# Kernel tuning notes

Measured on AMD Instinct MI355X. Metric: run time of the kernel, lower is better.

## Reference

```python
import jax, jax.numpy as jnp
import numpy as np
from jax import lax

# dims (see shape_source)
B, T = 256, 32
DQ, K, S, CTX = 128, 8, 4, 16
D = 2 * DQ + 1            # state_flat = [q (DQ), p (DQ), extra (1)]
EVO, DT, DAMP, TAU = 8, 0.2, 0.1, 1.0
TOPK = 2
GAMMA = 10.0              # gamma_pred
EPS = 1e-8


def _router(q, ctx, Wq, Wc, b):
    # chart routing: softmax over K charts, temperature TAU
    return jax.nn.softmax((q @ Wq + ctx @ Wc + b) / TAU, axis=-1)


def _decode_topk(x, w, rw, rb):
    # x: [B,D], w: [B,K] chart weights -> [B,S] logits via top-k chart mixture
    logits_k = jnp.einsum('bd,kvd->bkv', x, rw) + rb          # [B,K,S]
    wv, idx = lax.top_k(w, TOPK)
    wn = wv / jnp.clip(wv.sum(-1, keepdims=True), EPS)
    wm = jnp.zeros_like(w).at[jnp.arange(w.shape[0])[:, None], idx].set(wn)
    return jnp.einsum('bkv,bk->bv', logits_k, wm)


def setup_inputs() -> dict:
    key = jax.random.key(0)
    ks = jax.random.split(key, 11)
    return {
        'inputs': jax.random.randint(ks[0], (B, T), 0, 2),
        'targets': jax.random.randint(ks[1], (B, T), 0, S),
        'task_ids': jax.random.randint(ks[2], (B, T), 0, 2),
        'initial_state_flat': jax.random.normal(ks[3], (B, D), jnp.float32),
        'bit_embed': jax.random.normal(ks[4], (2, DQ), jnp.float32),
        'task_u_embed': jax.random.normal(ks[5], (2, DQ), jnp.float32),
        'router_ctx_embed': jax.random.normal(ks[6], (2, CTX), jnp.float32),
        'readout_weight': 0.1 * jax.random.normal(ks[7], (K, S, D), jnp.float32),
        'readout_bias': jnp.zeros((K, S), jnp.float32),
        'router_Wq': 0.1 * jax.random.normal(ks[8], (DQ, K), jnp.float32),
        'router_Wc': 0.1 * jax.random.normal(ks[9], (CTX, K), jnp.float32),
        'router_b': jnp.zeros((K,), jnp.float32),
        'A': 0.02 * jax.random.normal(ks[10], (K, DQ, DQ), jnp.float32),
    }


def reference(inputs, targets, task_ids, initial_state_flat, bit_embed, task_u_embed,
              router_ctx_embed, readout_weight, readout_bias, router_Wq, router_Wc,
              router_b, A):
    Bn, Tn = inputs.shape
    rows = jnp.arange(Bn)
    targets_prev = jnp.concatenate([jnp.zeros_like(targets[:, :1]), targets[:, :-1]], axis=1)

    def step(carry, xs):
        state, tF, tacc, tce, usage, tsum, tcnt, scw, scnt = carry
        bit_t, target_t, prev_t, task_t = xs
        u = jnp.tanh(bit_embed[bit_t]) + jnp.tanh(task_u_embed[task_t])   # [B,DQ]
        ctx = jnp.tanh(router_ctx_embed[task_t])                          # [B,CTX]

        def evo(st, _):
            q, p, s = st[:, :DQ], st[:, DQ:2 * DQ], st[:, 2 * DQ:]
            w = _router(q, ctx, router_Wq, router_Wc, router_b)           # [B,K]
            # chart-weighted mixture-of-experts dynamics (semi-implicit, damped)
            force = jnp.einsum('bk,kij,bj->bi', w, A, jnp.tanh(q))
            p_new = (1.0 - DT * DAMP) * p + DT * (force + u)
            q_new = q + DT * jnp.tanh(p_new)
            return jnp.concatenate([q_new, p_new, s], axis=1), w

        state, ws = lax.scan(evo, state, None, length=EVO)
        chart_w = ws[-1]                                                  # router w from last evo step
        q = state[:, :DQ]
        chart_w_next = _router(q, ctx, router_Wq, router_Wc, router_b)
        logits = _decode_topk(state, chart_w_next, readout_weight, readout_bias)  # [B,S]
        logits2 = logits[:, :2]
        tgt2 = jnp.where(task_t == 0, target_t, 0)
        ce2 = -jax.nn.log_softmax(logits2, axis=-1)[rows, tgt2]
        ce4 = -jax.nn.log_softmax(logits, axis=-1)[rows, target_t]
        mask2 = (task_t == 0).astype(jnp.float32)
        pred_error = mask2 * ce2 + (1.0 - mask2) * ce4
        chart_state_loss = -jnp.log(jnp.clip(chart_w, EPS))[rows, prev_t]
        F_t = GAMMA * (pred_error + chart_state_loss)

        pred = jnp.where(task_t == 0, jnp.argmax(logits2, -1), jnp.argmax(logits, -1))
        correct = (pred == target_t).astype(jnp.float32)
        task_oh = jax.nn.one_hot(task_t, 2, dtype=jnp.float32)
        mask4 = (task_t == 1).astype(jnp.float32)[:, None]
        state_oh = jax.nn.one_hot(prev_t, S, dtype=jnp.float32)
        carry = (state,
                 tF + F_t.mean(),
                 tacc + correct.mean(),
                 tce + pred_error.mean(),
                 usage + chart_w.sum(0),
                 tsum + (correct[:, None] * task_oh).sum(0),
                 tcnt + task_oh.sum(0),
                 scw + (state_oh * mask4).T @ chart_w,
                 scnt + (state_oh * mask4).sum(0))
        return carry, None

    zf = jnp.zeros((), jnp.float32)
    init = (initial_state_flat, zf, zf, zf,
            jnp.zeros((K,), jnp.float32), jnp.zeros((2,), jnp.float32),
            jnp.zeros((2,), jnp.float32), jnp.zeros((S, K), jnp.float32),
            jnp.zeros((S,), jnp.float32))
    xs = (inputs.T, targets.T, targets_prev.T, task_ids.T)
    (state, tF, tacc, tce, usage, tsum, tcnt, scw, scnt), _ = lax.scan(step, init, xs)

    mean_F = tF / Tn
    mean_acc = tacc / Tn
    mean_ce = tce / Tn
    per_task_acc = tsum / (tcnt + EPS)
    dist = usage / (usage.sum() + EPS)
    chart_ent = -(dist * jnp.log(dist + EPS)).sum()
    joint = scw / (scw.sum() + EPS)
    p_s = joint.sum(1, keepdims=True)
    p_c = joint.sum(0, keepdims=True)
    mi = (joint * (jnp.log(joint + EPS) - jnp.log(p_s + EPS) - jnp.log(p_c + EPS))).sum()
    mi = jnp.where(scw.sum() > 0, jnp.clip(mi, 0.0), 0.0)
    return (mean_F, mean_acc, mean_ce, usage, chart_ent, per_task_acc, scw, scnt, mi)
```

## Files before the change

### kernel.cpp

```cpp
#include <hip/hip_runtime.h>
#include <hip/hip_fp16.h>

namespace {
constexpr int kT = 32, kDQ = 128, kK = 8, kS = 4, kCTX = 16, kD = 257, kEVO = 8;
constexpr float kDT = 0.2f, kDAMP = 0.1f, kGAMMA = 10.0f, kEPS = 1e-8f;

typedef _Float16 h2 __attribute__((ext_vector_type(2)));

__device__ __forceinline__ float dot2h(unsigned a, unsigned b, float c) {
#if __has_builtin(__builtin_amdgcn_fdot2)
  return __builtin_amdgcn_fdot2(__builtin_bit_cast(h2, a), __builtin_bit_cast(h2, b), c, false);
#else
  h2 ha = __builtin_bit_cast(h2, a), hb = __builtin_bit_cast(h2, b);
  return c + (float)ha.x * (float)hb.x + (float)ha.y * (float)hb.y;
#endif
}

__device__ __forceinline__ unsigned packh2(float lo, float hi) {
  __half l = __float2half(lo), h = __float2half(hi);
  return (unsigned)__half_as_ushort(l) | ((unsigned)__half_as_ushort(h) << 16);
}
}

extern "C" __global__ void __launch_bounds__(1024)
seq_main(const int* __restrict__ inputs, const int* __restrict__ targets,
         const int* __restrict__ task_ids, const float* __restrict__ st0,
         const float* __restrict__ bit_emb, const float* __restrict__ task_u,
         const float* __restrict__ ctx_emb, const float* __restrict__ rw_g,
         const float* __restrict__ rb_g, const float* __restrict__ Wq_g,
         const float* __restrict__ Wc_g, const float* __restrict__ b_g,
         const float* __restrict__ A_g, float* __restrict__ ws) {
  const int tid = threadIdx.x;
  const int b = blockIdx.x;
  const int kq = tid >> 7, iq = tid & 127;

  __shared__ __align__(16) float q_l[kDQ];
  __shared__ __align__(16) float p_l[kDQ];
  __shared__ __align__(16) float u4_l[4][kDQ];
  __shared__ __align__(16) unsigned tq_l[kDQ / 2];
  __shared__ __align__(16) float Ybuf[kK][kDQ];
  __shared__ __align__(16) float Wq_l[kK][kDQ];
  __shared__ float wq_ctx2[2][kK];
  __shared__ float wlog_l[kK];
  __shared__ float w_l[kK];
  __shared__ float chartw_l[kK];
  __shared__ float rw_l[kK * kS * kD];
  __shared__ float rb_l[kK * kS];
  __shared__ float lk_l[kK * kS];
  __shared__ float acc_l[64];
  __shared__ float s_l;

  for (int idx = tid; idx < kK * kS * kD; idx += 1024) rw_l[idx] = rw_g[idx];
  if (tid < kDQ * kK) { int j = tid >> 3, kk = tid & 7; Wq_l[kk][j] = Wq_g[tid]; }
  if (tid < kK * kS) rb_l[tid] = rb_g[tid];
  if (tid < kDQ) { q_l[tid] = st0[b * kD + tid]; p_l[tid] = st0[b * kD + kDQ + tid]; }
  if (tid == 0) s_l = st0[b * kD + 2 * kDQ];
  if (tid < 64) acc_l[tid] = 0.f;
  if (tid < 512) {
    int cb = tid >> 7, i = tid & 127;
    u4_l[cb][i] = tanhf(bit_emb[(cb & 1) * kDQ + i]) + tanhf(task_u[(cb >> 1) * kDQ + i]);
  }
  if (tid < 16) {
    int tk = tid >> 3, kk = tid & 7;
    float s = b_g[kk];
    #pragma unroll
    for (int c = 0; c < kCTX; c++) s += tanhf(ctx_emb[tk * kCTX + c]) * Wc_g[c * kK + kk];
    wq_ctx2[tk][kk] = s;
  }
  unsigned a_[64];
  {
    const float4* Arow = reinterpret_cast<const float4*>(A_g + ((size_t)(kq * kDQ + iq)) * kDQ);
    #pragma unroll
    for (int jj = 0; jj < 32; jj++) {
      float4 f = Arow[jj];
      a_[2 * jj] = packh2(f.x, f.y);
      a_[2 * jj + 1] = packh2(f.z, f.w);
    }
  }
  __syncthreads();

  if (tid < kDQ) {
    float tv = tanhf(q_l[tid]);
    float to = __shfl_xor(tv, 1);
    if (!(tid & 1)) tq_l[tid >> 1] = packh2(tv, to);
  }
  if (tid < 512) {
    int kk = tid >> 6, l = tid & 63;
    float2 qp = reinterpret_cast<const float2*>(q_l)[l];
    float2 wp = reinterpret_cast<const float2*>(&Wq_l[kk][0])[l];
    float part = qp.x * wp.x + qp.y * wp.y;
    part += __shfl_xor(part, 1);  part += __shfl_xor(part, 2);
    part += __shfl_xor(part, 4);  part += __shfl_xor(part, 8);
    part += __shfl_xor(part, 16); part += __shfl_xor(part, 32);
    if (l == 0) wlog_l[kk] = part;
  }
  __syncthreads();

  const int boff = b * kT;
  for (int t = 0; t < kT; t++) {
    const int bit = inputs[boff + t];
    const int task = task_ids[boff + t];
    const int uix = task * 2 + bit;

    for (int e = 0; e < kEVO; e++) {
      if (tid < kK) {
        float myl = wlog_l[tid] + wq_ctx2[task][tid];
        float mx = myl;
        #pragma unroll
        for (int kk = 0; kk < kK; kk++) mx = fmaxf(mx, wlog_l[kk] + wq_ctx2[task][kk]);
        float ev = expf(myl - mx);
        float sm = ev;
        sm += __shfl_xor(sm, 1); sm += __shfl_xor(sm, 2); sm += __shfl_xor(sm, 4);
        w_l[tid] = ev / sm;
      }
      float y = 0.f;
      {
        const uint4* tq4 = reinterpret_cast<const uint4*>(tq_l);
        #pragma unroll
        for (int jj = 0; jj < 16; jj++) {
          uint4 tt = tq4[jj];
          y = dot2h(a_[4 * jj + 0], tt.x, y);
          y = dot2h(a_[4 * jj + 1], tt.y, y);
          y = dot2h(a_[4 * jj + 2], tt.z, y);
          y = dot2h(a_[4 * jj + 3], tt.w, y);
        }
      }
      Ybuf[kq][iq] = y;
      __syncthreads();
      if (tid < kDQ) {
        float f = 0.f;
        #pragma unroll
        for (int kk = 0; kk < kK; kk++) f += w_l[kk] * Ybuf[kk][tid];
        float pv = (1.f - kDT * kDAMP) * p_l[tid] + kDT * (f + u4_l[uix][tid]);
        float qv = q_l[tid] + kDT * tanhf(pv);
        p_l[tid] = pv; q_l[tid] = qv;
        float tv = tanhf(qv);
        float to = __shfl_xor(tv, 1);
        if (!(tid & 1)) tq_l[tid >> 1] = packh2(tv, to);
        if (e == kEVO - 1 && tid < kK) chartw_l[tid] = w_l[tid];
      }
      __syncthreads();
      if (tid < 512) {
        int kk = tid >> 6, l = tid & 63;
        float2 qp = reinterpret_cast<const float2*>(q_l)[l];
        float2 wp = reinterpret_cast<const float2*>(&Wq_l[kk][0])[l];
        float part = qp.x * wp.x + qp.y * wp.y;
        part += __shfl_xor(part, 1);  part += __shfl_xor(part, 2);
        part += __shfl_xor(part, 4);  part += __shfl_xor(part, 8);
        part += __shfl_xor(part, 16); part += __shfl_xor(part, 32);
        if (l == 0) wlog_l[kk] = part;
      }
      __syncthreads();
    }

    {
      int pair = tid >> 5, ln = tid & 31;
      const float* rwrow = &rw_l[pair * kD];
      float sacc = 0.f;
      #pragma unroll
      for (int m = 0; m < 8; m++) {
        int d = ln + 32 * m;
        float sv = (m < 4) ? q_l[d] : p_l[d - kDQ];
        sacc += sv * rwrow[d];
      }
      if (ln == 0) sacc += s_l * rwrow[256];
      sacc += __shfl_xor(sacc, 1); sacc += __shfl_xor(sacc, 2);
      sacc += __shfl_xor(sacc, 4); sacc += __shfl_xor(sacc, 8);
      sacc += __shfl_xor(sacc, 16);
      if (ln == 0) lk_l[pair] = sacc + rb_l[pair];
    }
    __syncthreads();
    if (tid == 0) {
      const int tgt = targets[boff + t];
      const int prv = (t == 0) ? 0 : targets[boff + t - 1];
      float lg[kK]; float mx = -1e30f;
      #pragma unroll
      for (int kk = 0; kk < kK; kk++) { lg[kk] = wlog_l[kk] + wq_ctx2[task][kk]; mx = fmaxf(mx, lg[kk]); }
      float cw[kK]; float ssum = 0.f;
      #pragma unroll
      for (int kk = 0; kk < kK; kk++) { cw[kk] = expf(lg[kk] - mx); ssum += cw[kk]; }
      float invs = 1.f / ssum;
      #pragma unroll
      for (int kk = 0; kk < kK; kk++) cw[kk] *= invs;
      int i0 = 0; float v0 = cw[0];
      #pragma unroll
      for (int kk = 1; kk < kK; kk++) if (cw[kk] > v0) { v0 = cw[kk]; i0 = kk; }
      int i1 = (i0 == 0) ? 1 : 0; float v1 = cw[i1];
      #pragma unroll
      for (int kk = 0; kk < kK; kk++) if (kk != i0 && cw[kk] > v1) { v1 = cw[kk]; i1 = kk; }
      float wsum = fmaxf(v0 + v1, kEPS);
      float wn0 = v0 / wsum, wn1 = v1 / wsum;
      float lg4[4];
      #pragma unroll
      for (int v = 0; v < 4; v++) lg4[v] = wn0 * lk_l[i0 * 4 + v] + wn1 * lk_l[i1 * 4 + v];
      float m2 = fmaxf(lg4[0], lg4[1]);
      float lse2 = m2 + logf(expf(lg4[0] - m2) + expf(lg4[1] - m2));
      float m4 = fmaxf(fmaxf(lg4[0], lg4[1]), fmaxf(lg4[2], lg4[3]));
      float lse4 = m4 + logf(expf(lg4[0] - m4) + expf(lg4[1] - m4) + expf(lg4[2] - m4) + expf(lg4[3] - m4));
      int idx2 = (tgt < 1) ? tgt : 1;
      float p2 = (idx2 == 0) ? lg4[0] : lg4[1];
      float p4 = (tgt == 0) ? lg4[0] : ((tgt == 1) ? lg4[1] : ((tgt == 2) ? lg4[2] : lg4[3]));
      float ce2 = lse2 - p2, ce4 = lse4 - p4;
      float pe = (task == 0) ? ce2 : ce4;
      int pred;
      if (task == 0) pred = (lg4[1] > lg4[0]) ? 1 : 0;
      else {
        pred = 0; float bv = lg4[0];
        if (lg4[1] > bv) { bv = lg4[1]; pred = 1; }
        if (lg4[2] > bv) { bv = lg4[2]; pred = 2; }
        if (lg4[3] > bv) { bv = lg4[3]; pred = 3; }
      }
      float corr = (pred == tgt) ? 1.f : 0.f;
      float csl = -logf(fmaxf(chartw_l[prv], kEPS));
      float Ft = kGAMMA * (pe + csl);
      acc_l[0] += Ft; acc_l[1] += corr; acc_l[2] += pe;
      #pragma unroll
      for (int kk = 0; kk < kK; kk++) acc_l[3 + kk] += chartw_l[kk];
      acc_l[11 + task] += corr; acc_l[13 + task] += 1.f;
      if (task == 1) {
        #pragma unroll
        for (int kk = 0; kk < kK; kk++) acc_l[15 + prv * kK + kk] += chartw_l[kk];
        acc_l[47 + prv] += 1.f;
      }
    }
    __syncthreads();
  }

  __syncthreads();
  if (tid < 64) ws[b * 64 + tid] = acc_l[tid];
}

extern "C" __global__ void seq_finalize(const float* __restrict__ ws, float* __restrict__ out) {
  const int tid = threadIdx.x;
  __shared__ float red[51];
  if (tid < 51) {
    float s = 0.f;
    for (int b = 0; b < 256; b++) s += ws[b * 64 + tid];
    red[tid] = s;
  }
  __syncthreads();
  if (tid == 0) {
    const float BT = 256.f * 32.f;
    out[0] = red[0] / BT;
    out[1] = red[1] / BT;
    out[2] = red[2] / BT;
    float us = 0.f;
    for (int k = 0; k < 8; k++) { out[3 + k] = red[3 + k]; us += red[3 + k]; }
    float ent = 0.f;
    for (int k = 0; k < 8; k++) {
      float dist = red[3 + k] / (us + kEPS);
      ent -= dist * logf(dist + kEPS);
    }
    out[11] = ent;
    out[12] = red[11] / (red[13] + kEPS);
    out[13] = red[12] / (red[14] + kEPS);
    float tot = 0.f;
    for (int j = 0; j < 32; j++) { out[14 + j] = red[15 + j]; tot += red[15 + j]; }
    for (int s2 = 0; s2 < 4; s2++) out[46 + s2] = red[47 + s2];
    float inv = 1.f / (tot + kEPS);
    float ps[4] = {0.f, 0.f, 0.f, 0.f};
    float pc[8] = {0.f, 0.f, 0.f, 0.f, 0.f, 0.f, 0.f, 0.f};
    for (int s2 = 0; s2 < 4; s2++)
      for (int k = 0; k < 8; k++) {
        float jv = red[15 + s2 * 8 + k] * inv;
        ps[s2] += jv; pc[k] += jv;
      }
    float mi = 0.f;
    for (int s2 = 0; s2 < 4; s2++)
      for (int k = 0; k < 8; k++) {
        float jv = red[15 + s2 * 8 + k] * inv;
        mi += jv * (logf(jv + kEPS) - logf(ps[s2] + kEPS) - logf(pc[k] + kEPS));
      }
    mi = (tot > 0.f) ? fmaxf(mi, 0.f) : 0.f;
    out[50] = mi;
  }
}

extern "C" void kernel_launch(void* const* d_in, const int* in_sizes, int n_in,
                              void* d_out, int out_size, void* d_ws, size_t ws_size,
                              hipStream_t stream) {
  (void)in_sizes; (void)n_in; (void)out_size; (void)ws_size;
  const int* inputs   = (const int*)d_in[0];
  const int* targets  = (const int*)d_in[1];
  const int* task_ids = (const int*)d_in[2];
  const float* st0      = (const float*)d_in[3];
  const float* bit_emb  = (const float*)d_in[4];
  const float* task_u   = (const float*)d_in[5];
  const float* ctx_emb  = (const float*)d_in[6];
  const float* rw       = (const float*)d_in[7];
  const float* rb       = (const float*)d_in[8];
  const float* Wq       = (const float*)d_in[9];
  const float* Wc       = (const float*)d_in[10];
  const float* bb       = (const float*)d_in[11];
  const float* A        = (const float*)d_in[12];
  float* ws  = (float*)d_ws;
  float* out = (float*)d_out;
  hipLaunchKernelGGL(seq_main, dim3(256), dim3(1024), 0, stream,
                     inputs, targets, task_ids, st0, bit_emb, task_u, ctx_emb,
                     rw, rb, Wq, Wc, bb, A, ws);
  hipLaunchKernelGGL(seq_finalize, dim3(1), dim3(64), 0, stream, ws, out);
}
```

Measured before the change: 441.6 us.

## Compute chart force matvecs with MFMA and keep per-lane state in registers

```diff
diff --git a/kernel.cpp b/kernel.cpp
--- a/kernel.cpp
+++ b/kernel.cpp
@@ -5,20 +5,17 @@
 constexpr int kT = 32, kDQ = 128, kK = 8, kS = 4, kCTX = 16, kD = 257, kEVO = 8;
 constexpr float kDT = 0.2f, kDAMP = 0.1f, kGAMMA = 10.0f, kEPS = 1e-8f;
 
-typedef _Float16 h2 __attribute__((ext_vector_type(2)));
-
-__device__ __forceinline__ float dot2h(unsigned a, unsigned b, float c) {
-#if __has_builtin(__builtin_amdgcn_fdot2)
-  return __builtin_amdgcn_fdot2(__builtin_bit_cast(h2, a), __builtin_bit_cast(h2, b), c, false);
-#else
-  h2 ha = __builtin_bit_cast(h2, a), hb = __builtin_bit_cast(h2, b);
-  return c + (float)ha.x * (float)hb.x + (float)ha.y * (float)hb.y;
-#endif
-}
+typedef _Float16 half8 __attribute__((ext_vector_type(8)));
+typedef float f32x4 __attribute__((ext_vector_type(4)));
+typedef unsigned u32x4 __attribute__((ext_vector_type(4)));
 
 __device__ __forceinline__ unsigned packh2(float lo, float hi) {
   __half l = __float2half(lo), h = __float2half(hi);
   return (unsigned)__half_as_ushort(l) | ((unsigned)__half_as_ushort(h) << 16);
+}
+__device__ __forceinline__ float fast_tanh(float x) {
+  float e = __expf(2.f * x);
+  return 1.f - 2.f / (e + 1.f);
 }
 }
 
@@ -30,30 +27,27 @@
          const float* __restrict__ rb_g, const float* __restrict__ Wq_g,
          const float* __restrict__ Wc_g, const float* __restrict__ b_g,
          const float* __restrict__ A_g, float* __restrict__ ws) {
-  const int tid = threadIdx.x;
-  const int b = blockIdx.x;
-  const int kq = tid >> 7, iq = tid & 127;
-
+  const int tid = threadIdx.x, b = blockIdx.x;
+  const int lane = tid & 63, w = tid >> 6;
+  const int il = lane & 7;
+  const int own_i = 8 * w + il;
+  const int g4 = lane >> 4;
+
+  __shared__ __align__(16) float rw_l[kK * kS * kD];
+  __shared__ __align__(16) float u4_l[4][kDQ];
   __shared__ __align__(16) float q_l[kDQ];
   __shared__ __align__(16) float p_l[kDQ];
-  __shared__ __align__(16) float u4_l[4][kDQ];
-  __shared__ __align__(16) unsigned tq_l[kDQ / 2];
-  __shared__ __align__(16) float Ybuf[kK][kDQ];
-  __shared__ __align__(16) float Wq_l[kK][kDQ];
-  __shared__ float wq_ctx2[2][kK];
-  __shared__ float wlog_l[kK];
-  __shared__ float w_l[kK];
-  __shared__ float chartw_l[kK];
-  __shared__ float rw_l[kK * kS * kD];
+  __shared__ __align__(16) unsigned tq_l[2][64];
+  __shared__ __align__(16) float wq_ctx2[2][kK];
+  __shared__ __align__(16) float wlog_l[kK];
+  __shared__ __align__(16) float chartw_l[kK];
   __shared__ float rb_l[kK * kS];
   __shared__ float lk_l[kK * kS];
   __shared__ float acc_l[64];
   __shared__ float s_l;
 
   for (int idx = tid; idx < kK * kS * kD; idx += 1024) rw_l[idx] = rw_g[idx];
-  if (tid < kDQ * kK) { int j = tid >> 3, kk = tid & 7; Wq_l[kk][j] = Wq_g[tid]; }
   if (tid < kK * kS) rb_l[tid] = rb_g[tid];
-  if (tid < kDQ) { q_l[tid] = st0[b * kD + tid]; p_l[tid] = st0[b * kD + kDQ + tid]; }
   if (tid == 0) s_l = st0[b * kD + 2 * kDQ];
   if (tid < 64) acc_l[tid] = 0.f;
   if (tid < 512) {
@@ -67,89 +61,129 @@
     for (int c = 0; c < kCTX; c++) s += tanhf(ctx_emb[tk * kCTX + c]) * Wc_g[c * kK + kk];
     wq_ctx2[tk][kk] = s;
   }
-  unsigned a_[64];
+  float wpx = 0.f, wpy = 0.f;
+  if (tid < 512) {
+    int kk = tid >> 6, l2 = tid & 63;
+    wpx = Wq_g[(2 * l2) * kK + kk];
+    wpy = Wq_g[(2 * l2 + 1) * kK + kk];
+  }
+
+  const int kA = (lane & 3) + 4 * ((lane >> 3) & 1);
+  const int ipar = (lane >> 2) & 1;
+  u32x4 afr[4][4];
+  #pragma unroll
+  for (int mt = 0; mt < 4; mt++) {
+    const float* arow = A_g + ((size_t)kA * kDQ + (8 * w + 2 * mt + ipar)) * kDQ;
+    #pragma unroll
+    for (int ks = 0; ks < 4; ks++) {
+      const float4* p4 = reinterpret_cast<const float4*>(arow + 32 * ks + 8 * g4);
+      float4 f0 = p4[0], f1 = p4[1];
+      u32x4 v;
+      v.x = packh2(f0.x, f0.y); v.y = packh2(f0.z, f0.w);
+      v.z = packh2(f1.x, f1.y); v.w = packh2(f1.z, f1.w);
+      afr[mt][ks] = v;
+    }
+  }
+
+  float q = st0[b * kD + own_i];
+  float p = st0[b * kD + kDQ + own_i];
+  float tv = fast_tanh(q);
+
+  if (lane < 8) q_l[own_i] = q;
   {
-    const float4* Arow = reinterpret_cast<const float4*>(A_g + ((size_t)(kq * kDQ + iq)) * kDQ);
-    #pragma unroll
-    for (int jj = 0; jj < 32; jj++) {
-      float4 f = Arow[jj];
-      a_[2 * jj] = packh2(f.x, f.y);
-      a_[2 * jj + 1] = packh2(f.z, f.w);
-    }
+    float to = __shfl_xor(tv, 1);
+    if (lane < 8 && !(lane & 1)) tq_l[0][4 * w + (lane >> 1)] = packh2(tv, to);
   }
   __syncthreads();
-
-  if (tid < kDQ) {
-    float tv = tanhf(q_l[tid]);
-    float to = __shfl_xor(tv, 1);
-    if (!(tid & 1)) tq_l[tid >> 1] = packh2(tv, to);
-  }
   if (tid < 512) {
-    int kk = tid >> 6, l = tid & 63;
-    float2 qp = reinterpret_cast<const float2*>(q_l)[l];
-    float2 wp = reinterpret_cast<const float2*>(&Wq_l[kk][0])[l];
-    float part = qp.x * wp.x + qp.y * wp.y;
+    int kk = tid >> 6, l2 = tid & 63;
+    float2 qp = reinterpret_cast<const float2*>(q_l)[l2];
+    float part = qp.x * wpx + qp.y * wpy;
     part += __shfl_xor(part, 1);  part += __shfl_xor(part, 2);
     part += __shfl_xor(part, 4);  part += __shfl_xor(part, 8);
     part += __shfl_xor(part, 16); part += __shfl_xor(part, 32);
-    if (l == 0) wlog_l[kk] = part;
+    if (l2 == 0) wlog_l[kk] = part;
   }
   __syncthreads();
 
+  const bool selb1 = ((lane >> 1) & 1) != 0;
+  const bool selb2 = ((lane >> 2) & 1) != 0;
+  const bool selp  = (((lane & 1) ^ ((lane >> 4) & 1)) != 0);
+  const bool hsel  = ((lane >> 5) & 1) != 0;
+
+  int sb = 0;
   const int boff = b * kT;
   for (int t = 0; t < kT; t++) {
     const int bit = inputs[boff + t];
     const int task = task_ids[boff + t];
-    const int uix = task * 2 + bit;
+    const float u_own = u4_l[task * 2 + bit][own_i];
+    f32x4 ctxA, ctxB;
+    {
+      const f32x4* cp = reinterpret_cast<const f32x4*>(&wq_ctx2[task][0]);
+      ctxA = cp[0]; ctxB = cp[1];
+    }
 
     for (int e = 0; e < kEVO; e++) {
-      if (tid < kK) {
-        float myl = wlog_l[tid] + wq_ctx2[task][tid];
-        float mx = myl;
-        #pragma unroll
-        for (int kk = 0; kk < kK; kk++) mx = fmaxf(mx, wlog_l[kk] + wq_ctx2[task][kk]);
-        float ev = expf(myl - mx);
-        float sm = ev;
-        sm += __shfl_xor(sm, 1); sm += __shfl_xor(sm, 2); sm += __shfl_xor(sm, 4);
-        w_l[tid] = ev / sm;
-      }
-      float y = 0.f;
-      {
-        const uint4* tq4 = reinterpret_cast<const uint4*>(tq_l);
-        #pragma unroll
-        for (int jj = 0; jj < 16; jj++) {
-          uint4 tt = tq4[jj];
-          y = dot2h(a_[4 * jj + 0], tt.x, y);
-          y = dot2h(a_[4 * jj + 1], tt.y, y);
-          y = dot2h(a_[4 * jj + 2], tt.z, y);
-          y = dot2h(a_[4 * jj + 3], tt.w, y);
-        }
-      }
-      Ybuf[kq][iq] = y;
-      __syncthreads();
-      if (tid < kDQ) {
-        float f = 0.f;
-        #pragma unroll
-        for (int kk = 0; kk < kK; kk++) f += w_l[kk] * Ybuf[kk][tid];
-        float pv = (1.f - kDT * kDAMP) * p_l[tid] + kDT * (f + u4_l[uix][tid]);
-        float qv = q_l[tid] + kDT * tanhf(pv);
-        p_l[tid] = pv; q_l[tid] = qv;
-        float tv = tanhf(qv);
-        float to = __shfl_xor(tv, 1);
-        if (!(tid & 1)) tq_l[tid >> 1] = packh2(tv, to);
-        if (e == kEVO - 1 && tid < kK) chartw_l[tid] = w_l[tid];
+      const f32x4* wl4 = reinterpret_cast<const f32x4*>(wlog_l);
+      f32x4 lgA = wl4[0] + ctxA, lgB = wl4[1] + ctxB;
+      float mx = fmaxf(fmaxf(fmaxf(lgA.x, lgA.y), fmaxf(lgA.z, lgA.w)),
+                       fmaxf(fmaxf(lgB.x, lgB.y), fmaxf(lgB.z, lgB.w)));
+      float e0 = __expf(lgA.x - mx), e1 = __expf(lgA.y - mx);
+      float e2 = __expf(lgA.z - mx), e3 = __expf(lgA.w - mx);
+      float e4 = __expf(lgB.x - mx), e5 = __expf(lgB.y - mx);
+      float e6 = __expf(lgB.z - mx), e7 = __expf(lgB.w - mx);
+      float inv = 1.f / (e0 + e1 + e2 + e3 + e4 + e5 + e6 + e7);
+      float w0 = e0 * inv, w1 = e1 * inv, w2 = e2 * inv, w3 = e3 * inv;
+      float w4 = e4 * inv, w5 = e5 * inv, w6 = e6 * inv, w7 = e7 * inv;
+      float ws0 = hsel ? w4 : w0, ws1 = hsel ? w5 : w1;
+      float ws2 = hsel ? w6 : w2, ws3 = hsel ? w7 : w3;
+
+      const u32x4* tq4 = reinterpret_cast<const u32x4*>(tq_l[sb]);
+      f32x4 ac0 = {0.f, 0.f, 0.f, 0.f}, ac1 = ac0, ac2 = ac0, ac3 = ac0;
+      #pragma unroll
+      for (int ks = 0; ks < 4; ks++) {
+        half8 bf = __builtin_bit_cast(half8, tq4[4 * ks + g4]);
+        ac0 = __builtin_amdgcn_mfma_f32_16x16x32_f16(__builtin_bit_cast(half8, afr[0][ks]), bf, ac0, 0, 0, 0);
+        ac1 = __builtin_amdgcn_mfma_f32_16x16x32_f16(__builtin_bit_cast(half8, afr[1][ks]), bf, ac1, 0, 0, 0);
+        ac2 = __builtin_amdgcn_mfma_f32_16x16x32_f16(__builtin_bit_cast(half8, afr[2][ks]), bf, ac2, 0, 0, 0);
+        ac3 = __builtin_amdgcn_mfma_f32_16x16x32_f16(__builtin_bit_cast(half8, afr[3][ks]), bf, ac3, 0, 0, 0);
+      }
+      float f0 = ws0 * ac0.x + ws1 * ac0.y + ws2 * ac0.z + ws3 * ac0.w;
+      float f1 = ws0 * ac1.x + ws1 * ac1.y + ws2 * ac1.z + ws3 * ac1.w;
+      float f2 = ws0 * ac2.x + ws1 * ac2.y + ws2 * ac2.z + ws3 * ac2.w;
+      float f3 = ws0 * ac3.x + ws1 * ac3.y + ws2 * ac3.z + ws3 * ac3.w;
+      f0 += __shfl_xor(f0, 32); f1 += __shfl_xor(f1, 32);
+      f2 += __shfl_xor(f2, 32); f3 += __shfl_xor(f3, 32);
+      float sA = selb2 ? (selb1 ? f3 : f2) : (selb1 ? f1 : f0);
+      float sB = __shfl_xor(sA, 16);
+      float force = selp ? sB : sA;
+
+      float pn = (1.f - kDT * kDAMP) * p + kDT * (force + u_own);
+      float tvp = fast_tanh(pn);
+      q = q + kDT * tvp;
+      p = pn;
+      tv = fast_tanh(q);
+      float to = __shfl_xor(tv, 1);
+      if (lane < 8) {
+        q_l[own_i] = q;
+        if (!(lane & 1)) tq_l[sb ^ 1][4 * w + (lane >> 1)] = packh2(tv, to);
+        if (e == kEVO - 1) p_l[own_i] = p;
+      }
+      if (e == kEVO - 1 && tid == 0) {
+        chartw_l[0] = w0; chartw_l[1] = w1; chartw_l[2] = w2; chartw_l[3] = w3;
+        chartw_l[4] = w4; chartw_l[5] = w5; chartw_l[6] = w6; chartw_l[7] = w7;
       }
       __syncthreads();
       if (tid < 512) {
-        int kk = tid >> 6, l = tid & 63;
-        float2 qp = reinterpret_cast<const float2*>(q_l)[l];
-        float2 wp = reinterpret_cast<const float2*>(&Wq_l[kk][0])[l];
-        float part = qp.x * wp.x + qp.y * wp.y;
+        int kk = tid >> 6, l2 = tid & 63;
+        float2 qp = reinterpret_cast<const float2*>(q_l)[l2];
+        float part = qp.x * wpx + qp.y * wpy;
         part += __shfl_xor(part, 1);  part += __shfl_xor(part, 2);
         part += __shfl_xor(part, 4);  part += __shfl_xor(part, 8);
         part += __shfl_xor(part, 16); part += __shfl_xor(part, 32);
-        if (l == 0) wlog_l[kk] = part;
-      }
+        if (l2 == 0) wlog_l[kk] = part;
+      }
+      sb ^= 1;
       __syncthreads();
     }
 
@@ -199,8 +233,8 @@
       float lse4 = m4 + logf(expf(lg4[0] - m4) + expf(lg4[1] - m4) + expf(lg4[2] - m4) + expf(lg4[3] - m4));
       int idx2 = (tgt < 1) ? tgt : 1;
       float p2 = (idx2 == 0) ? lg4[0] : lg4[1];
-      float p4 = (tgt == 0) ? lg4[0] : ((tgt == 1) ? lg4[1] : ((tgt == 2) ? lg4[2] : lg4[3]));
-      float ce2 = lse2 - p2, ce4 = lse4 - p4;
+      float p4v = (tgt == 0) ? lg4[0] : ((tgt == 1) ? lg4[1] : ((tgt == 2) ? lg4[2] : lg4[3]));
+      float ce2 = lse2 - p2, ce4 = lse4 - p4v;
       float pe = (task == 0) ? ce2 : ce4;
       int pred;
       if (task == 0) pred = (lg4[1] > lg4[0]) ? 1 : 0;
@@ -226,7 +260,6 @@
     __syncthreads();
   }
 
-  __syncthreads();
   if (tid < 64) ws[b * 64 + tid] = acc_l[tid];
 }
 
```

Result: slower. 532.1 us (+20.5%).

## Restructure recurrent kernel into single-barrier steps with register-resident state and fused routing

Applied to the files above, without the earlier changes.

```diff
diff --git a/kernel.cpp b/kernel.cpp
--- a/kernel.cpp
+++ b/kernel.cpp
@@ -2,12 +2,17 @@
 #include <hip/hip_fp16.h>
 
 namespace {
-constexpr int kT = 32, kDQ = 128, kK = 8, kS = 4, kCTX = 16, kD = 257, kEVO = 8;
+constexpr int kT = 32, kDQ = 128, kK = 8, kD = 257, kCTX = 16;
 constexpr float kDT = 0.2f, kDAMP = 0.1f, kGAMMA = 10.0f, kEPS = 1e-8f;
 
 typedef _Float16 h2 __attribute__((ext_vector_type(2)));
-
-__device__ __forceinline__ float dot2h(unsigned a, unsigned b, float c) {
+typedef __fp16 fp16x2 __attribute__((ext_vector_type(2)));
+
+__device__ __forceinline__ unsigned pk16(float lo, float hi) {
+  fp16x2 r = __builtin_amdgcn_cvt_pkrtz(lo, hi);
+  return __builtin_bit_cast(unsigned, r);
+}
+__device__ __forceinline__ float dot2(unsigned a, unsigned b, float c) {
 #if __has_builtin(__builtin_amdgcn_fdot2)
   return __builtin_amdgcn_fdot2(__builtin_bit_cast(h2, a), __builtin_bit_cast(h2, b), c, false);
 #else
@@ -15,219 +20,266 @@
   return c + (float)ha.x * (float)hb.x + (float)ha.y * (float)hb.y;
 #endif
 }
-
-__device__ __forceinline__ unsigned packh2(float lo, float hi) {
-  __half l = __float2half(lo), h = __float2half(hi);
-  return (unsigned)__half_as_ushort(l) | ((unsigned)__half_as_ushort(h) << 16);
-}
-}
-
-extern "C" __global__ void __launch_bounds__(1024)
+__device__ __forceinline__ float fast_tanh(float x) {
+  float e = __expf(2.f * x);
+  return 1.f - 2.f / (e + 1.f);
+}
+}
+
+extern "C" __global__ void __launch_bounds__(512, 2)
 seq_main(const int* __restrict__ inputs, const int* __restrict__ targets,
          const int* __restrict__ task_ids, const float* __restrict__ st0,
          const float* __restrict__ bit_emb, const float* __restrict__ task_u,
          const float* __restrict__ ctx_emb, const float* __restrict__ rw_g,
          const float* __restrict__ rb_g, const float* __restrict__ Wq_g,
          const float* __restrict__ Wc_g, const float* __restrict__ b_g,
-         const float* __restrict__ A_g, float* __restrict__ ws) {
-  const int tid = threadIdx.x;
-  const int b = blockIdx.x;
-  const int kq = tid >> 7, iq = tid & 127;
-
-  __shared__ __align__(16) float q_l[kDQ];
-  __shared__ __align__(16) float p_l[kDQ];
+         const float* __restrict__ A_g, float* __restrict__ wsout) {
+  const int tid = threadIdx.x, b = blockIdx.x;
+  const int w = tid >> 6, lane = tid & 63;
+  const int k = lane >> 3, il = lane & 7;
+  const int i0 = 8 * w + il;
+
+  __shared__ __align__(16) unsigned tq_l[2][64];
+  __shared__ __align__(16) unsigned q16_l[2][64];
+  __shared__ __align__(16) unsigned p16_l[64];
+  __shared__ __align__(16) unsigned rw16_l[32][132];
   __shared__ __align__(16) float u4_l[4][kDQ];
-  __shared__ __align__(16) unsigned tq_l[kDQ / 2];
-  __shared__ __align__(16) float Ybuf[kK][kDQ];
-  __shared__ __align__(16) float Wq_l[kK][kDQ];
-  __shared__ float wq_ctx2[2][kK];
-  __shared__ float wlog_l[kK];
-  __shared__ float w_l[kK];
-  __shared__ float chartw_l[kK];
-  __shared__ float rw_l[kK * kS * kD];
-  __shared__ float rb_l[kK * kS];
-  __shared__ float lk_l[kK * kS];
+  __shared__ float rws_l[32], rb_l[32];
+  __shared__ float chartw_l[kK], cwnext_l[kK];
+  __shared__ float lk_l[32];
   __shared__ float acc_l[64];
-  __shared__ float s_l;
-
-  for (int idx = tid; idx < kK * kS * kD; idx += 1024) rw_l[idx] = rw_g[idx];
-  if (tid < kDQ * kK) { int j = tid >> 3, kk = tid & 7; Wq_l[kk][j] = Wq_g[tid]; }
-  if (tid < kK * kS) rb_l[tid] = rb_g[tid];
-  if (tid < kDQ) { q_l[tid] = st0[b * kD + tid]; p_l[tid] = st0[b * kD + kDQ + tid]; }
-  if (tid == 0) s_l = st0[b * kD + 2 * kDQ];
+  __shared__ int task_l[kT], sel_l[kT], tgt_l[kT];
+
   if (tid < 64) acc_l[tid] = 0.f;
-  if (tid < 512) {
+  if (tid < 32) { rws_l[tid] = rw_g[tid * kD + 256]; rb_l[tid] = rb_g[tid]; }
+  if (tid >= 64 && tid < 96) {
+    int t = tid - 64;
+    int bit = inputs[b * kT + t];
+    int task = task_ids[b * kT + t];
+    task_l[t] = task; sel_l[t] = task * 2 + bit; tgt_l[t] = targets[b * kT + t];
+  }
+  {
     int cb = tid >> 7, i = tid & 127;
     u4_l[cb][i] = tanhf(bit_emb[(cb & 1) * kDQ + i]) + tanhf(task_u[(cb >> 1) * kDQ + i]);
   }
-  if (tid < 16) {
-    int tk = tid >> 3, kk = tid & 7;
-    float s = b_g[kk];
-    #pragma unroll
-    for (int c = 0; c < kCTX; c++) s += tanhf(ctx_emb[tk * kCTX + c]) * Wc_g[c * kK + kk];
-    wq_ctx2[tk][kk] = s;
-  }
-  unsigned a_[64];
+  for (int idx = tid; idx < 32 * 128; idx += 512) {
+    int pr = idx >> 7, dw = idx & 127;
+    rw16_l[pr][dw] = pk16(rw_g[pr * kD + 2 * dw], rw_g[pr * kD + 2 * dw + 1]);
+  }
+
+  unsigned a0_[64], a1_[64];
   {
-    const float4* Arow = reinterpret_cast<const float4*>(A_g + ((size_t)(kq * kDQ + iq)) * kDQ);
-    #pragma unroll
-    for (int jj = 0; jj < 32; jj++) {
-      float4 f = Arow[jj];
-      a_[2 * jj] = packh2(f.x, f.y);
-      a_[2 * jj + 1] = packh2(f.z, f.w);
-    }
-  }
+    const float4* r0 = (const float4*)(A_g + ((size_t)(k * kDQ + i0)) * kDQ);
+    const float4* r1 = (const float4*)(A_g + ((size_t)(k * kDQ + i0 + 64)) * kDQ);
+    #pragma unroll
+    for (int jj = 0; jj < 32; ++jj) {
+      float4 f = r0[jj];
+      a0_[2 * jj] = pk16(f.x, f.y); a0_[2 * jj + 1] = pk16(f.z, f.w);
+      f = r1[jj];
+      a1_[2 * jj] = pk16(f.x, f.y); a1_[2 * jj + 1] = pk16(f.z, f.w);
+    }
+  }
+  unsigned wqh[8];
+  #pragma unroll
+  for (int m = 0; m < 8; ++m)
+    wqh[m] = pk16(Wq_g[(16 * il + 2 * m) * kK + k], Wq_g[(16 * il + 2 * m + 1) * kK + k]);
+  float ctx0k = b_g[k], ctx1k = b_g[k];
+  #pragma unroll
+  for (int c = 0; c < kCTX; ++c) {
+    float wc = Wc_g[c * kK + k];
+    ctx0k += tanhf(ctx_emb[c]) * wc;
+    ctx1k += tanhf(ctx_emb[kCTX + c]) * wc;
+  }
+  const float s_f = st0[b * kD + 256];
+
+  float q0 = st0[b * kD + i0],        p0 = st0[b * kD + kDQ + i0];
+  float q1 = st0[b * kD + i0 + 64],   p1 = st0[b * kD + kDQ + i0 + 64];
+  {
+    float tv0 = fast_tanh(q0), tv1 = fast_tanh(q1);
+    float qo0 = __shfl_xor(q0, 1), qo1 = __shfl_xor(q1, 1);
+    float to0 = __shfl_xor(tv0, 1), to1 = __shfl_xor(tv1, 1);
+    if (lane < 8 && !(il & 1)) {
+      int dw = 4 * w + (il >> 1);
+      q16_l[0][dw] = pk16(q0, qo0);       tq_l[0][dw] = pk16(tv0, to0);
+      q16_l[0][32 + dw] = pk16(q1, qo1);  tq_l[0][32 + dw] = pk16(tv1, to1);
+    }
+  }
+  float u0 = 0.f, u1 = 0.f;
   __syncthreads();
 
-  if (tid < kDQ) {
-    float tv = tanhf(q_l[tid]);
-    float to = __shfl_xor(tv, 1);
-    if (!(tid & 1)) tq_l[tid >> 1] = packh2(tv, to);
-  }
-  if (tid < 512) {
-    int kk = tid >> 6, l = tid & 63;
-    float2 qp = reinterpret_cast<const float2*>(q_l)[l];
-    float2 wp = reinterpret_cast<const float2*>(&Wq_l[kk][0])[l];
-    float part = qp.x * wp.x + qp.y * wp.y;
-    part += __shfl_xor(part, 1);  part += __shfl_xor(part, 2);
-    part += __shfl_xor(part, 4);  part += __shfl_xor(part, 8);
-    part += __shfl_xor(part, 16); part += __shfl_xor(part, 32);
-    if (l == 0) wlog_l[kk] = part;
+  auto runDecode = [&]() {
+    int pair = tid >> 4, ln = tid & 15;
+    uint4 sa, sb;
+    if (ln < 8) {
+      sa = ((const uint4*)q16_l[0])[2 * ln]; sb = ((const uint4*)q16_l[0])[2 * ln + 1];
+    } else {
+      sa = ((const uint4*)p16_l)[2 * (ln - 8)]; sb = ((const uint4*)p16_l)[2 * (ln - 8) + 1];
+    }
+    uint4 ra = ((const uint4*)&rw16_l[pair][0])[2 * ln];
+    uint4 rb2 = ((const uint4*)&rw16_l[pair][0])[2 * ln + 1];
+    float d = 0.f;
+    d = dot2(sa.x, ra.x, d); d = dot2(sa.y, ra.y, d);
+    d = dot2(sa.z, ra.z, d); d = dot2(sa.w, ra.w, d);
+    d = dot2(sb.x, rb2.x, d); d = dot2(sb.y, rb2.y, d);
+    d = dot2(sb.z, rb2.z, d); d = dot2(sb.w, rb2.w, d);
+    if (ln == 0) d += s_f * rws_l[pair];
+    d += __shfl_xor(d, 1); d += __shfl_xor(d, 2);
+    d += __shfl_xor(d, 4); d += __shfl_xor(d, 8);
+    if (ln == 0) lk_l[pair] = d + rb_l[pair];
+  };
+
+  auto runTail = [&](int t) {
+    if (tid != 0) return;
+    const int tgt = tgt_l[t];
+    const int task = task_l[t];
+    const int prv = (t == 0) ? 0 : tgt_l[t - 1];
+    float cw[kK], ch[kK];
+    #pragma unroll
+    for (int kk = 0; kk < kK; ++kk) { cw[kk] = cwnext_l[kk]; ch[kk] = chartw_l[kk]; }
+    int i0_ = 0; float v0 = cw[0];
+    #pragma unroll
+    for (int kk = 1; kk < kK; ++kk) if (cw[kk] > v0) { v0 = cw[kk]; i0_ = kk; }
+    int i1_ = (i0_ == 0) ? 1 : 0; float v1 = (i0_ == 0) ? cw[1] : cw[0];
+    #pragma unroll
+    for (int kk = 0; kk < kK; ++kk) if (kk != i0_ && cw[kk] > v1) { v1 = cw[kk]; i1_ = kk; }
+    float wsum = fmaxf(v0 + v1, kEPS);
+    float wn0 = v0 / wsum, wn1 = v1 / wsum;
+    float lg4[4];
+    #pragma unroll
+    for (int v = 0; v < 4; ++v) lg4[v] = wn0 * lk_l[i0_ * 4 + v] + wn1 * lk_l[i1_ * 4 + v];
+    float m2 = fmaxf(lg4[0], lg4[1]);
+    float lse2 = m2 + logf(expf(lg4[0] - m2) + expf(lg4[1] - m2));
+    float m4 = fmaxf(fmaxf(lg4[0], lg4[1]), fmaxf(lg4[2], lg4[3]));
+    float lse4 = m4 + logf(expf(lg4[0] - m4) + expf(lg4[1] - m4) +
+                           expf(lg4[2] - m4) + expf(lg4[3] - m4));
+    int idx2 = (tgt < 1) ? tgt : 1;
+    float p2 = (idx2 == 0) ? lg4[0] : lg4[1];
+    float p4v = (tgt == 0) ? lg4[0] : ((tgt == 1) ? lg4[1] : ((tgt == 2) ? lg4[2] : lg4[3]));
+    float pe = (task == 0) ? (lse2 - p2) : (lse4 - p4v);
+    int pred;
+    if (task == 0) pred = (lg4[1] > lg4[0]) ? 1 : 0;
+    else {
+      pred = 0; float bv = lg4[0];
+      if (lg4[1] > bv) { bv = lg4[1]; pred = 1; }
+      if (lg4[2] > bv) { bv = lg4[2]; pred = 2; }
+      if (lg4[3] > bv) { bv = lg4[3]; pred = 3; }
+    }
+    float corr = (pred == tgt) ? 1.f : 0.f;
+    float csl = -logf(fmaxf(ch[prv], kEPS));
+    acc_l[0] += kGAMMA * (pe + csl); acc_l[1] += corr; acc_l[2] += pe;
+    #pragma unroll
+    for (int kk = 0; kk < kK; ++kk) acc_l[3 + kk] += ch[kk];
+    acc_l[11 + task] += corr; acc_l[13 + task] += 1.f;
+    if (task == 1) {
+      #pragma unroll
+      for (int kk = 0; kk < kK; ++kk) acc_l[15 + prv * kK + kk] += ch[kk];
+      acc_l[47 + prv] += 1.f;
+    }
+  };
+
+  #pragma unroll 1
+  for (int s = 0; s < 256; ++s) {
+    const int cb = s & 1, nb = cb ^ 1;
+    const int e = s & 7, t = s >> 3;
+
+    uint4 qa = ((const uint4*)q16_l[cb])[2 * il];
+    uint4 qb = ((const uint4*)q16_l[cb])[2 * il + 1];
+    float rl = 0.f;
+    rl = dot2(wqh[0], qa.x, rl); rl = dot2(wqh[1], qa.y, rl);
+    rl = dot2(wqh[2], qa.z, rl); rl = dot2(wqh[3], qa.w, rl);
+    rl = dot2(wqh[4], qb.x, rl); rl = dot2(wqh[5], qb.y, rl);
+    rl = dot2(wqh[6], qb.z, rl); rl = dot2(wqh[7], qb.w, rl);
+    rl += __shfl_xor(rl, 1); rl += __shfl_xor(rl, 2); rl += __shfl_xor(rl, 4);
+
+    if (e == 0) {
+      if (s != 0) {
+        float lgp = rl + (task_l[t - 1] ? ctx1k : ctx0k);
+        float mxp = lgp;
+        mxp = fmaxf(mxp, __shfl_xor(mxp, 8));
+        mxp = fmaxf(mxp, __shfl_xor(mxp, 16));
+        mxp = fmaxf(mxp, __shfl_xor(mxp, 32));
+        float exp_ = __expf(lgp - mxp);
+        float smp = exp_;
+        smp += __shfl_xor(smp, 8); smp += __shfl_xor(smp, 16); smp += __shfl_xor(smp, 32);
+        if (w == 0 && il == 0) cwnext_l[k] = exp_ / smp;
+        runDecode();
+      }
+      int sel = sel_l[t];
+      u0 = u4_l[sel][i0]; u1 = u4_l[sel][i0 + 64];
+    }
+    if (e == 1 && s > 8) runTail(t - 1);
+
+    float lg = rl + (task_l[t] ? ctx1k : ctx0k);
+    float mx = lg;
+    mx = fmaxf(mx, __shfl_xor(mx, 8));
+    mx = fmaxf(mx, __shfl_xor(mx, 16));
+    mx = fmaxf(mx, __shfl_xor(mx, 32));
+    float ex = __expf(lg - mx);
+    float sm = ex;
+    sm += __shfl_xor(sm, 8); sm += __shfl_xor(sm, 16); sm += __shfl_xor(sm, 32);
+    float wk = ex / sm;
+    if (e == 7 && w == 0 && il == 0) chartw_l[k] = wk;
+
+    float y0a = 0.f, y0b = 0.f, y0c = 0.f, y0d = 0.f;
+    float y1a = 0.f, y1b = 0.f, y1c = 0.f, y1d = 0.f;
+    const uint4* tq4 = (const uint4*)tq_l[cb];
+    #pragma unroll
+    for (int jj = 0; jj < 16; ++jj) {
+      uint4 tt = tq4[jj];
+      y0a = dot2(a0_[4 * jj + 0], tt.x, y0a); y0b = dot2(a0_[4 * jj + 1], tt.y, y0b);
+      y0c = dot2(a0_[4 * jj + 2], tt.z, y0c); y0d = dot2(a0_[4 * jj + 3], tt.w, y0d);
+      y1a = dot2(a1_[4 * jj + 0], tt.x, y1a); y1b = dot2(a1_[4 * jj + 1], tt.y, y1b);
+      y1c = dot2(a1_[4 * jj + 2], tt.z, y1c); y1d = dot2(a1_[4 * jj + 3], tt.w, y1d);
+    }
+    float f0 = wk * ((y0a + y0b) + (y0c + y0d));
+    float f1 = wk * ((y1a + y1b) + (y1c + y1d));
+    f0 += __shfl_xor(f0, 8); f0 += __shfl_xor(f0, 16); f0 += __shfl_xor(f0, 32);
+    f1 += __shfl_xor(f1, 8); f1 += __shfl_xor(f1, 16); f1 += __shfl_xor(f1, 32);
+
+    float pn0 = (1.f - kDT * kDAMP) * p0 + kDT * (f0 + u0);
+    float pn1 = (1.f - kDT * kDAMP) * p1 + kDT * (f1 + u1);
+    q0 += kDT * fast_tanh(pn0); p0 = pn0;
+    q1 += kDT * fast_tanh(pn1); p1 = pn1;
+    float tv0 = fast_tanh(q0), tv1 = fast_tanh(q1);
+    float qo0 = __shfl_xor(q0, 1), qo1 = __shfl_xor(q1, 1);
+    float to0 = __shfl_xor(tv0, 1), to1 = __shfl_xor(tv1, 1);
+    float po0 = __shfl_xor(p0, 1), po1 = __shfl_xor(p1, 1);
+    if (lane < 8 && !(il & 1)) {
+      int dw = 4 * w + (il >> 1);
+      q16_l[nb][dw] = pk16(q0, qo0);       tq_l[nb][dw] = pk16(tv0, to0);
+      q16_l[nb][32 + dw] = pk16(q1, qo1);  tq_l[nb][32 + dw] = pk16(tv1, to1);
+      if (e == 7) {
+        p16_l[dw] = pk16(p0, po0);
+        p16_l[32 + dw] = pk16(p1, po1);
+      }
+    }
+    __syncthreads();
+  }
+
+  {
+    uint4 qa = ((const uint4*)q16_l[0])[2 * il];
+    uint4 qb = ((const uint4*)q16_l[0])[2 * il + 1];
+    float rl = 0.f;
+    rl = dot2(wqh[0], qa.x, rl); rl = dot2(wqh[1], qa.y, rl);
+    rl = dot2(wqh[2], qa.z, rl); rl = dot2(wqh[3], qa.w, rl);
+    rl = dot2(wqh[4], qb.x, rl); rl = dot2(wqh[5], qb.y, rl);
+    rl = dot2(wqh[6], qb.z, rl); rl = dot2(wqh[7], qb.w, rl);
+    rl += __shfl_xor(rl, 1); rl += __shfl_xor(rl, 2); rl += __shfl_xor(rl, 4);
+    float lgp = rl + (task_l[31] ? ctx1k : ctx0k);
+    float mxp = lgp;
+    mxp = fmaxf(mxp, __shfl_xor(mxp, 8));
+    mxp = fmaxf(mxp, __shfl_xor(mxp, 16));
+    mxp = fmaxf(mxp, __shfl_xor(mxp, 32));
+    float exp_ = __expf(lgp - mxp);
+    float smp = exp_;
+    smp += __shfl_xor(smp, 8); smp += __shfl_xor(smp, 16); smp += __shfl_xor(smp, 32);
+    if (w == 0 && il == 0) cwnext_l[k] = exp_ / smp;
+    runDecode();
   }
   __syncthreads();
-
-  const int boff = b * kT;
-  for (int t = 0; t < kT; t++) {
-    const int bit = inputs[boff + t];
-    const int task = task_ids[boff + t];
-    const int uix = task * 2 + bit;
-
-    for (int e = 0; e < kEVO; e++) {
-      if (tid < kK) {
-        float myl = wlog_l[tid] + wq_ctx2[task][tid];
-        float mx = myl;
-        #pragma unroll
-        for (int kk = 0; kk < kK; kk++) mx = fmaxf(mx, wlog_l[kk] + wq_ctx2[task][kk]);
-        float ev = expf(myl - mx);
-        float sm = ev;
-        sm += __shfl_xor(sm, 1); sm += __shfl_xor(sm, 2); sm += __shfl_xor(sm, 4);
-        w_l[tid] = ev / sm;
-      }
-      float y = 0.f;
-      {
-        const uint4* tq4 = reinterpret_cast<const uint4*>(tq_l);
-        #pragma unroll
-        for (int jj = 0; jj < 16; jj++) {
-          uint4 tt = tq4[jj];
-          y = dot2h(a_[4 * jj + 0], tt.x, y);
-          y = dot2h(a_[4 * jj + 1], tt.y, y);
-          y = dot2h(a_[4 * jj + 2], tt.z, y);
-          y = dot2h(a_[4 * jj + 3], tt.w, y);
-        }
-      }
-      Ybuf[kq][iq] = y;
-      __syncthreads();
-      if (tid < kDQ) {
-        float f = 0.f;
-        #pragma unroll
-        for (int kk = 0; kk < kK; kk++) f += w_l[kk] * Ybuf[kk][tid];
-        float pv = (1.f - kDT * kDAMP) * p_l[tid] + kDT * (f + u4_l[uix][tid]);
-        float qv = q_l[tid] + kDT * tanhf(pv);
-        p_l[tid] = pv; q_l[tid] = qv;
-        float tv = tanhf(qv);
-        float to = __shfl_xor(tv, 1);
-        if (!(tid & 1)) tq_l[tid >> 1] = packh2(tv, to);
-        if (e == kEVO - 1 && tid < kK) chartw_l[tid] = w_l[tid];
-      }
-      __syncthreads();
-      if (tid < 512) {
-        int kk = tid >> 6, l = tid & 63;
-        float2 qp = reinterpret_cast<const float2*>(q_l)[l];
-        float2 wp = reinterpret_cast<const float2*>(&Wq_l[kk][0])[l];
-        float part = qp.x * wp.x + qp.y * wp.y;
-        part += __shfl_xor(part, 1);  part += __shfl_xor(part, 2);
-        part += __shfl_xor(part, 4);  part += __shfl_xor(part, 8);
-        part += __shfl_xor(part, 16); part += __shfl_xor(part, 32);
-        if (l == 0) wlog_l[kk] = part;
-      }
-      __syncthreads();
-    }
-
-    {
-      int pair = tid >> 5, ln = tid & 31;
-      const float* rwrow = &rw_l[pair * kD];
-      float sacc = 0.f;
-      #pragma unroll
-      for (int m = 0; m < 8; m++) {
-        int d = ln + 32 * m;
-        float sv = (m < 4) ? q_l[d] : p_l[d - kDQ];
-        sacc += sv * rwrow[d];
-      }
-      if (ln == 0) sacc += s_l * rwrow[256];
-      sacc += __shfl_xor(sacc, 1); sacc += __shfl_xor(sacc, 2);
-      sacc += __shfl_xor(sacc, 4); sacc += __shfl_xor(sacc, 8);
-      sacc += __shfl_xor(sacc, 16);
-      if (ln == 0) lk_l[pair] = sacc + rb_l[pair];
-    }
-    __syncthreads();
-    if (tid == 0) {
-      const int tgt = targets[boff + t];
-      const int prv = (t == 0) ? 0 : targets[boff + t - 1];
-      float lg[kK]; float mx = -1e30f;
-      #pragma unroll
-      for (int kk = 0; kk < kK; kk++) { lg[kk] = wlog_l[kk] + wq_ctx2[task][kk]; mx = fmaxf(mx, lg[kk]); }
-      float cw[kK]; float ssum = 0.f;
-      #pragma unroll
-      for (int kk = 0; kk < kK; kk++) { cw[kk] = expf(lg[kk] - mx); ssum += cw[kk]; }
-      float invs = 1.f / ssum;
-      #pragma unroll
-      for (int kk = 0; kk < kK; kk++) cw[kk] *= invs;
-      int i0 = 0; float v0 = cw[0];
-      #pragma unroll
-      for (int kk = 1; kk < kK; kk++) if (cw[kk] > v0) { v0 = cw[kk]; i0 = kk; }
-      int i1 = (i0 == 0) ? 1 : 0; float v1 = cw[i1];
-      #pragma unroll
-      for (int kk = 0; kk < kK; kk++) if (kk != i0 && cw[kk] > v1) { v1 = cw[kk]; i1 = kk; }
-      float wsum = fmaxf(v0 + v1, kEPS);
-      float wn0 = v0 / wsum, wn1 = v1 / wsum;
-      float lg4[4];
-      #pragma unroll
-      for (int v = 0; v < 4; v++) lg4[v] = wn0 * lk_l[i0 * 4 + v] + wn1 * lk_l[i1 * 4 + v];
-      float m2 = fmaxf(lg4[0], lg4[1]);
-      float lse2 = m2 + logf(expf(lg4[0] - m2) + expf(lg4[1] - m2));
-      float m4 = fmaxf(fmaxf(lg4[0], lg4[1]), fmaxf(lg4[2], lg4[3]));
-      float lse4 = m4 + logf(expf(lg4[0] - m4) + expf(lg4[1] - m4) + expf(lg4[2] - m4) + expf(lg4[3] - m4));
-      int idx2 = (tgt < 1) ? tgt : 1;
-      float p2 = (idx2 == 0) ? lg4[0] : lg4[1];
-      float p4 = (tgt == 0) ? lg4[0] : ((tgt == 1) ? lg4[1] : ((tgt == 2) ? lg4[2] : lg4[3]));
-      float ce2 = lse2 - p2, ce4 = lse4 - p4;
-      float pe = (task == 0) ? ce2 : ce4;
-      int pred;
-      if (task == 0) pred = (lg4[1] > lg4[0]) ? 1 : 0;
-      else {
-        pred = 0; float bv = lg4[0];
-        if (lg4[1] > bv) { bv = lg4[1]; pred = 1; }
-        if (lg4[2] > bv) { bv = lg4[2]; pred = 2; }
-        if (lg4[3] > bv) { bv = lg4[3]; pred = 3; }
-      }
-      float corr = (pred == tgt) ? 1.f : 0.f;
-      float csl = -logf(fmaxf(chartw_l[prv], kEPS));
-      float Ft = kGAMMA * (pe + csl);
-      acc_l[0] += Ft; acc_l[1] += corr; acc_l[2] += pe;
-      #pragma unroll
-      for (int kk = 0; kk < kK; kk++) acc_l[3 + kk] += chartw_l[kk];
-      acc_l[11 + task] += corr; acc_l[13 + task] += 1.f;
-      if (task == 1) {
-        #pragma unroll
-        for (int kk = 0; kk < kK; kk++) acc_l[15 + prv * kK + kk] += chartw_l[kk];
-        acc_l[47 + prv] += 1.f;
-      }
-    }
-    __syncthreads();
-  }
-
+  runTail(31);
   __syncthreads();
-  if (tid < 64) ws[b * 64 + tid] = acc_l[tid];
+  if (tid < 64) wsout[b * 64 + tid] = acc_l[tid];
 }
 
 extern "C" __global__ void seq_finalize(const float* __restrict__ ws, float* __restrict__ out) {
@@ -295,7 +347,7 @@
   const float* A        = (const float*)d_in[12];
   float* ws  = (float*)d_ws;
   float* out = (float*)d_out;
-  hipLaunchKernelGGL(seq_main, dim3(256), dim3(1024), 0, stream,
+  hipLaunchKernelGGL(seq_main, dim3(256), dim3(512), 0, stream,
                      inputs, targets, task_ids, st0, bit_emb, task_u, ctx_emb,
                      rw, rb, Wq, Wc, bb, A, ws);
   hipLaunchKernelGGL(seq_finalize, dim3(1), dim3(64), 0, stream, ws, out);
```

After: 515.3 us. 1.17x slower.
